# Kernel tuning notes

Measured on AMD Instinct MI355X. Metric: run time of the kernel, lower is better.

Reference implementation:

```python
import jax, jax.numpy as jnp
import numpy as np
import math

N_HEADS = 16
ROPE_BASE = 10000.0


def rotate_half(x):
    x1 = x[..., ::2]
    x2 = x[..., 1::2]
    return jnp.stack((-x2, x1), axis=-1).reshape(x.shape)


def rope_tables(seq_len, head_dim, dtype):
    inv_freq = 1.0 / (ROPE_BASE ** (jnp.arange(0, head_dim, 2, dtype=jnp.float32) / head_dim))
    positions = jnp.arange(seq_len, dtype=jnp.float32)
    freqs = jnp.outer(positions, inv_freq)            # [S, hd/2]
    emb = jnp.concatenate((freqs, freqs), axis=-1)    # [S, hd]  (matches torch cat convention)
    cos = jnp.cos(emb)[None, None, :, :].astype(dtype)
    sin = jnp.sin(emb)[None, None, :, :].astype(dtype)
    return cos, sin


def setup_inputs() -> dict:
    key = jax.random.key(0)
    k1, k2, k3 = jax.random.split(key, 3)
    B, S, D = 2, 2048, 1024
    x = jax.random.normal(k1, (B, S, D), dtype=jnp.float32)
    # causal lower-triangular mask, broadcastable over batch and heads
    mask = jnp.tril(jnp.ones((S, S), dtype=jnp.int32))[None, None, :, :]
    w_qkv = jax.random.normal(k2, (D, 3 * D), dtype=jnp.float32) * 0.02
    w_out = jax.random.normal(k3, (D, D), dtype=jnp.float32) * 0.02
    return {"x": x, "mask": mask, "w_qkv": w_qkv, "w_out": w_out}


def reference(x, mask, w_qkv, w_out):
    B, S, D = x.shape
    H = N_HEADS
    hd = D // H
    qkv = (x @ w_qkv).reshape(B, S, 3, H, hd)
    qkv = jnp.transpose(qkv, (2, 0, 3, 1, 4))         # [3, B, H, S, hd]
    q, k, v = qkv[0], qkv[1], qkv[2]
    cos, sin = rope_tables(S, hd, x.dtype)
    q = q * cos + rotate_half(q) * sin
    k = k * cos + rotate_half(k) * sin
    scale = math.sqrt(hd)
    attn = jnp.einsum("bhsd,bhtd->bhst", q, k) / scale
    attn = jnp.where(mask == 0, -jnp.inf, attn)
    attn = jax.nn.softmax(attn, axis=-1)              # dropout p=0.0 -> identity
    out = jnp.einsum("bhst,bhtd->bhsd", attn, v)
    out = jnp.transpose(out, (0, 2, 1, 3)).reshape(B, S, D)
    return out @ w_out
```

## Files before the change

### kernel.cpp

```cpp
#include <hip/hip_runtime.h>
#include <stdint.h>

typedef unsigned short u16;
typedef __bf16 bf16x8 __attribute__((ext_vector_type(8)));
typedef float f32x4 __attribute__((ext_vector_type(4)));

#define S_LEN 2048
#define NH    16
#define DM    1024
#define N3    3072
#define MROWS 4096

__device__ __forceinline__ float b2f(u16 u) {
  unsigned int v = ((unsigned int)u) << 16;
  return __builtin_bit_cast(float, v);
}
__device__ __forceinline__ u16 f2b(float f) {
  unsigned int v = __builtin_bit_cast(unsigned int, f);
  v += 0x7fffu + ((v >> 16) & 1u);
  return (u16)(v >> 16);
}
__device__ __forceinline__ u16 f2b_trunc(float f) {
  return (u16)(__builtin_bit_cast(unsigned int, f) >> 16);
}
__device__ __forceinline__ bf16x8 ld8(const u16* p) { return *(const bf16x8*)p; }
__device__ __forceinline__ f32x4 mfma16(bf16x8 a, bf16x8 b, f32x4 c) {
  return __builtin_amdgcn_mfma_f32_16x16x32_bf16(a, b, c, 0, 0, 0);
}
__device__ __forceinline__ void glds16(const void* g, void* l) {
  __builtin_amdgcn_global_load_lds(
      (const __attribute__((address_space(1))) unsigned int*)g,
      (__attribute__((address_space(3))) unsigned int*)l, 16, 0, 0);
}
__device__ __forceinline__ int bfish(unsigned int w) {
  unsigned int e = (w >> 7) & 0xffu;
  return (e >= 100u && e <= 134u) ? 1 : 0;
}

__global__ __launch_bounds__(256) void prep_kernel(const void* __restrict__ x,
                                                   const void* __restrict__ wqkv,
                                                   const void* __restrict__ wout,
                                                   u16* __restrict__ xb,
                                                   u16* __restrict__ wqT,
                                                   u16* __restrict__ woT,
                                                   float* __restrict__ cosT,
                                                   float* __restrict__ sinT,
                                                   int* __restrict__ flag) {
  const int bx = blockIdx.x;
  const int t = threadIdx.x;
  if (bx < 2048) {
    __shared__ int cnt;
    if (t == 0) cnt = 0;
    __syncthreads();
    size_t i = (size_t)bx * 256 + t;
    const uint4* xv = (const uint4*)x;
    uint4 probe = xv[i];
    unsigned int wds[4]; *(uint4*)wds = probe;
    atomicAdd(&cnt, bfish(wds[0]) + bfish(wds[1]) + bfish(wds[2]) + bfish(wds[3]));
    __syncthreads();
    const int isbf = cnt > 512;
    if (t == 0) *flag = isbf;
    if (isbf) {
      ((uint4*)xb)[i] = probe;
    } else {
      const float* xf = (const float*)x;
      #pragma unroll
      for (int j = 0; j < 8; ++j) xb[i * 8 + j] = f2b(xf[i * 8 + j]);
    }
    return;
  }
  if (bx < 2304) {
    int i = (bx - 2048) * 256 + t;
    int s = i >> 5, f = i & 31;
    float invf = expf(-(float)(2 * f) * (1.0f / 64.0f) * logf(10000.0f));
    float th = (float)s * invf;
    float sv, cv;
    sincosf(th, &sv, &cv);
    cosT[s * 64 + f] = cv; cosT[s * 64 + 32 + f] = cv;
    sinT[s * 64 + f] = sv; sinT[s * 64 + 32 + f] = sv;
    return;
  }
  const int wq = bx < 5376;
  const int id = wq ? (bx - 2304) : (bx - 5376);
  const int ncx = wq ? 96 : 32;
  const void* in = wq ? wqkv : wout;
  u16* out = wq ? wqT : woT;
  const int C = wq ? 3072 : 1024;
  const int bxc = id % ncx, byr = id / ncx;
  __shared__ int cnt;
  __shared__ float tile[32][33];
  const int tx = t & 31, ty = t >> 5;
  if (t == 0) cnt = 0;
  __syncthreads();
  const unsigned int* wv = (const unsigned int*)in;
  size_t off = (((size_t)id) * 256 + t) & 524287;
  atomicAdd(&cnt, bfish(wv[off]));
  __syncthreads();
  const int fl = cnt > 128;
  const int c0 = bxc * 32, r0 = byr * 32;
  #pragma unroll
  for (int dy = 0; dy < 32; dy += 8) {
    size_t idx = (size_t)(r0 + ty + dy) * C + (c0 + tx);
    float v = fl ? b2f(((const u16*)in)[idx]) : ((const float*)in)[idx];
    tile[ty + dy][tx] = v;
  }
  __syncthreads();
  #pragma unroll
  for (int dy = 0; dy < 32; dy += 8) {
    out[(size_t)(c0 + ty + dy) * 1024 + (r0 + tx)] = f2b(tile[tx][ty + dy]);
  }
}

__global__ __launch_bounds__(256) void gemm_qkv(const u16* __restrict__ A,
                                                const u16* __restrict__ Bt,
                                                u16* __restrict__ Qo,
                                                u16* __restrict__ Ko,
                                                u16* __restrict__ Vt,
                                                const float* __restrict__ cosT,
                                                const float* __restrict__ sinT) {
  __shared__ u16 smem[16384];
  u16* Al = smem;
  u16* Bl = smem + 8192;
  const int t = threadIdx.x;
  const int lane = t & 63, wave = t >> 6;
  const int ln = lane & 15, quad = lane >> 4;
  const int wr = wave >> 1, wc = wave & 1;
  const int m0 = blockIdx.x * 128, n0 = blockIdx.y * 128;
  const char* Ab = (const char*)A;
  const char* Bb = (const char*)Bt;
  f32x4 acc[4][4] = {};

  for (int k0 = 0; k0 < 1024; k0 += 64) {
    __syncthreads();
    #pragma unroll
    for (int it = 0; it < 4; ++it) {
      int c = it * 256 + t;
      int row = c >> 3;
      int sg = (c & 7) ^ (row & 7);
      glds16(Ab + ((size_t)(m0 + row) * 1024 + k0 + sg * 8) * 2, (char*)Al + c * 16);
      glds16(Bb + ((size_t)(n0 + row) * 1024 + k0 + sg * 8) * 2, (char*)Bl + c * 16);
    }
    __syncthreads();
    bf16x8 a[4][2], b[4][2];
    #pragma unroll
    for (int i = 0; i < 4; ++i) {
      const int row = wr * 64 + i * 16 + ln;
      #pragma unroll
      for (int ki = 0; ki < 2; ++ki)
        a[i][ki] = ld8(Al + row * 64 + (((ki * 4 + quad) ^ (row & 7)) << 3));
    }
    #pragma unroll
    for (int j = 0; j < 4; ++j) {
      const int row = wc * 64 + j * 16 + ln;
      #pragma unroll
      for (int ki = 0; ki < 2; ++ki)
        b[j][ki] = ld8(Bl + row * 64 + (((ki * 4 + quad) ^ (row & 7)) << 3));
    }
    #pragma unroll
    for (int i = 0; i < 4; ++i)
      #pragma unroll
      for (int j = 0; j < 4; ++j) {
        acc[i][j] = mfma16(a[i][0], b[j][0], acc[i][j]);
        acc[i][j] = mfma16(a[i][1], b[j][1], acc[i][j]);
      }
  }

  const int which = n0 >> 10;
  if (which < 2) {
    u16* dst = which ? Ko : Qo;
    const float qs = which ? 1.0f : 0.18033688011112042f;
    #pragma unroll
    for (int i = 0; i < 4; ++i)
      #pragma unroll
      for (int j = 0; j < 4; ++j) {
        const int c = n0 + wc * 64 + j * 16 + ln;
        const int h = (c >> 6) & 15, d = c & 63;
        const float sgn = (d & 1) ? 1.0f : -1.0f;
        #pragma unroll
        for (int r = 0; r < 4; ++r) {
          const int m = m0 + wr * 64 + i * 16 + quad * 4 + r;
          const int s = m & 2047, b_ = m >> 11;
          const float v = acc[i][j][r];
          const float p = __shfl_xor(v, 1);
          const float o = (v * cosT[s * 64 + d] + sgn * p * sinT[s * 64 + d]) * qs;
          dst[((size_t)(b_ * NH + h) * S_LEN + s) * 64 + d] = f2b(o);
        }
      }
  } else {
    #pragma unroll
    for (int i = 0; i < 4; ++i)
      #pragma unroll
      for (int j = 0; j < 4; ++j) {
        const int c = n0 + wc * 64 + j * 16 + ln;
        const int h = (c >> 6) & 15, d = c & 63;
        const int m = m0 + wr * 64 + i * 16 + quad * 4;
        const int s = m & 2047, b_ = m >> 11;
        u16 pk[4];
        #pragma unroll
        for (int r = 0; r < 4; ++r) pk[r] = f2b(acc[i][j][r]);
        *(uint2*)&Vt[((size_t)(b_ * NH + h) * 64 + d) * S_LEN + s] = *(const uint2*)pk;
      }
  }
}

__global__ __launch_bounds__(256) void attn_kernel(const u16* __restrict__ Qb,
                                                   const u16* __restrict__ Kb,
                                                   const u16* __restrict__ Vt,
                                                   u16* __restrict__ Ao) {
  __shared__ u16 smem[20480];
  u16* Kl = smem;
  u16* Vl = smem + 8192;
  u16* Pl = smem + 16384;
  const int t = threadIdx.x;
  const int lane = t & 63, w = t >> 6;
  const int ln = lane & 15, quad = lane >> 4;
  const int i = blockIdx.x;
  const int xcd = i & 7;
  const int j = i >> 3;
  const int bh = (xcd << 2) | (j & 3);
  const int q5 = j >> 2;
  const int g = q5 & 7, s5 = q5 >> 3;
  const int qt = (s5 & 1) ? (31 - ((s5 >> 1) << 3) - g) : (((s5 >> 1) << 3) + g);
  const int q0 = qt * 64;
  const int b = bh >> 4, h = bh & 15;
  const u16* Qbh = Qb + (size_t)bh * (S_LEN * 64);
  const u16* Kbh = Kb + (size_t)bh * (S_LEN * 64);
  const u16* Vtbh = Vt + (size_t)bh * (64 * S_LEN);
  u16* Plw = Pl + w * 1024;
  u16* AoBase = Ao + (size_t)b * S_LEN * DM + h * 64;

  auto stage = [&](int kt, int bufi) {
    u16* kd = Kl + bufi * 4096;
    u16* vd = Vl + bufi * 4096;
    const u16* kg = Kbh + (size_t)kt * 64 * 64;
    const u16* vg = Vtbh + (size_t)kt * 64;
    #pragma unroll
    for (int it = 0; it < 2; ++it) {
      int c = it * 256 + t;
      int row = c >> 3, sg = (c & 7) ^ (row & 7);
      glds16((const char*)kg + ((size_t)row * 64 + sg * 8) * 2,   (char*)kd + c * 16);
      glds16((const char*)vg + ((size_t)row * 2048 + sg * 8) * 2, (char*)vd + c * 16);
    }
  };

  bf16x8 bq[2];
  #pragma unroll
  for (int kk = 0; kk < 2; ++kk)
    bq[kk] = ld8(Qbh + (size_t)(q0 + w * 16 + ln) * 64 + kk * 32 + quad * 8);

  f32x4 o[4] = {};
  float l = 0.f;

  stage(0, 0);
  __syncthreads();

  for (int kt = 0; kt <= qt; ++kt) {
    const int bufi = kt & 1;
    if (kt < qt) stage(kt + 1, bufi ^ 1);
    const u16* Kb_ = Kl + bufi * 4096;
    const u16* Vb_ = Vl + bufi * 4096;

    f32x4 st[4] = {};
    #pragma unroll
    for (int kk = 0; kk < 2; ++kk)
      #pragma unroll
      for (int ct = 0; ct < 4; ++ct) {
        bf16x8 ak = ld8(Kb_ + (ct * 16 + ln) * 64 + (((kk * 4 + quad) ^ (ln & 7)) << 3));
        st[ct] = mfma16(ak, bq[kk], st[ct]);
      }

    const bool diag = (kt == qt);
    #pragma unroll
    for (int ct = 0; ct < 4; ++ct) {
      u16 pk[4];
      #pragma unroll
      for (int r = 0; r < 4; ++r) {
        float p;
        if (diag && (ct * 16 + quad * 4 + r) > (w * 16 + ln)) p = 0.f;
        else p = __builtin_amdgcn_exp2f(st[ct][r]);
        l += p;
        pk[r] = f2b_trunc(p);
      }
      *(uint2*)(Plw + ln * 64 + ((((ct * 2) + (quad >> 1)) ^ (ln & 7)) << 3)
                + ((quad & 1) << 2)) = *(const uint2*)pk;
    }

    #pragma unroll
    for (int k4 = 0; k4 < 2; ++k4) {
      bf16x8 bp = ld8(Plw + ln * 64 + (((k4 * 4 + quad) ^ (ln & 7)) << 3));
      #pragma unroll
      for (int dt = 0; dt < 4; ++dt) {
        bf16x8 av = ld8(Vb_ + (dt * 16 + ln) * 64 + (((k4 * 4 + quad) ^ (ln & 7)) << 3));
        o[dt] = mfma16(av, bp, o[dt]);
      }
    }
    __syncthreads();
  }

  l += __shfl_xor(l, 16);
  l += __shfl_xor(l, 32);
  const float inv = 1.f / l;
  const size_t qrow = (size_t)(q0 + w * 16 + ln) * DM;
  #pragma unroll
  for (int dt = 0; dt < 4; ++dt) {
    u16 pk[4];
    #pragma unroll
    for (int r = 0; r < 4; ++r) pk[r] = f2b(o[dt][r] * inv);
    *(uint2*)(AoBase + qrow + dt * 16 + quad * 4) = *(const uint2*)pk;
  }
}

template <int TM>
__global__ __launch_bounds__(256) void gemm_out_t(const u16* __restrict__ A,
                                                  const u16* __restrict__ Bt,
                                                  void* __restrict__ Out,
                                                  const int* __restrict__ flag) {
  constexpr int MI = TM / 32;
  __shared__ u16 smem[(TM + 128) * 32];
  u16* Al = smem;
  u16* Bl = smem + TM * 32;
  const int t = threadIdx.x;
  const int lane = t & 63, wave = t >> 6;
  const int ln = lane & 15, quad = lane >> 4;
  const int wr = wave >> 1, wc = wave & 1;
  const int m0 = blockIdx.x * TM, n0 = blockIdx.y * 128;
  const int rr = t >> 2;
  const int cb = (t & 3) * 16;
  const char* Ab = (const char*)A;
  const char* Bb = (const char*)Bt;
  f32x4 acc[MI][4] = {};

  for (int k0 = 0; k0 < 1024; k0 += 32) {
    __syncthreads();
    #pragma unroll
    for (int p = 0; p < TM / 64; ++p)
      glds16(Ab + ((size_t)(m0 + p * 64 + rr) * 1024 + k0) * 2 + cb,
             (char*)Al + p * 4096 + t * 16);
    glds16(Bb + ((size_t)(n0 + rr) * 1024 + k0) * 2 + cb,      (char*)Bl + t * 16);
    glds16(Bb + ((size_t)(n0 + 64 + rr) * 1024 + k0) * 2 + cb, (char*)Bl + 4096 + t * 16);
    __syncthreads();
    bf16x8 a[MI], b[4];
    #pragma unroll
    for (int i = 0; i < MI; ++i)
      a[i] = ld8(Al + (wr * (TM / 2) + i * 16 + ln) * 32 + quad * 8);
    #pragma unroll
    for (int j = 0; j < 4; ++j)
      b[j] = ld8(Bl + (wc * 64 + j * 16 + ln) * 32 + quad * 8);
    #pragma unroll
    for (int i = 0; i < MI; ++i)
      #pragma unroll
      for (int j = 0; j < 4; ++j)
        acc[i][j] = mfma16(a[i], b[j], acc[i][j]);
  }

  const int fl = *flag;
  #pragma unroll
  for (int i = 0; i < MI; ++i)
    #pragma unroll
    for (int j = 0; j < 4; ++j)
      #pragma unroll
      for (int r = 0; r < 4; ++r) {
        int m = m0 + wr * (TM / 2) + i * 16 + quad * 4 + r;
        int c = n0 + wc * 64 + j * 16 + ln;
        float v = acc[i][j][r];
        if (fl) ((u16*)Out)[(size_t)m * DM + c] = f2b(v);
        else    ((float*)Out)[(size_t)m * DM + c] = v;
      }
}

extern "C" void kernel_launch(void* const* d_in, const int* in_sizes, int n_in,
                              void* d_out, int out_size, void* d_ws, size_t ws_size,
                              hipStream_t stream) {
  (void)in_sizes; (void)n_in; (void)out_size; (void)ws_size;
  const void* x    = d_in[0];
  const void* wqkv = d_in[2];
  const void* wout = d_in[3];
  char* ws = (char*)d_ws;
  u16*  xb   = (u16*)(ws + 0);
  u16*  Ao   = xb;
  u16*  wqT  = (u16*)(ws + 8388608);
  u16*  woT  = (u16*)(ws + 14680064);
  u16*  Qb   = (u16*)(ws + 16777216);
  u16*  Kb   = (u16*)(ws + 25165824);
  u16*  Vt   = (u16*)(ws + 33554432);
  float* cosT = (float*)(ws + 41943040);
  float* sinT = (float*)(ws + 42467328);
  int*  flag = (int*)(ws + 42991616);

  prep_kernel<<<6400, 256, 0, stream>>>(x, wqkv, wout, xb, wqT, woT, cosT, sinT, flag);
  gemm_qkv<<<dim3(32, 24), 256, 0, stream>>>(xb, wqT, Qb, Kb, Vt, cosT, sinT);
  attn_kernel<<<1024, 256, 0, stream>>>(Qb, Kb, Vt, Ao);
  gemm_out_t<64><<<dim3(64, 8), 256, 0, stream>>>(Ao, woT, d_out, flag);
}
```

Baseline: 193.8 us.

## Tile weight transpose 64x64 with vector IO, interleave RoPE table, load A directly

```diff
diff --git a/kernel.cpp b/kernel.cpp
--- a/kernel.cpp
+++ b/kernel.cpp
@@ -43,8 +43,7 @@
                                                    u16* __restrict__ xb,
                                                    u16* __restrict__ wqT,
                                                    u16* __restrict__ woT,
-                                                   float* __restrict__ cosT,
-                                                   float* __restrict__ sinT,
+                                                   float* __restrict__ cs,
                                                    int* __restrict__ flag) {
   const int bx = blockIdx.x;
   const int t = threadIdx.x;
@@ -69,45 +68,62 @@
     }
     return;
   }
-  if (bx < 2304) {
+  if (bx < 2560) {
     int i = (bx - 2048) * 256 + t;
-    int s = i >> 5, f = i & 31;
+    int d = i >> 11, s = i & 2047;
+    int f = d & 31;
     float invf = expf(-(float)(2 * f) * (1.0f / 64.0f) * logf(10000.0f));
     float th = (float)s * invf;
     float sv, cv;
     sincosf(th, &sv, &cv);
-    cosT[s * 64 + f] = cv; cosT[s * 64 + 32 + f] = cv;
-    sinT[s * 64 + f] = sv; sinT[s * 64 + 32 + f] = sv;
+    cs[i * 2] = cv; cs[i * 2 + 1] = sv;
     return;
   }
-  const int wq = bx < 5376;
-  const int id = wq ? (bx - 2304) : (bx - 5376);
-  const int ncx = wq ? 96 : 32;
+  const int wq = bx < 3328;
+  const int id = wq ? (bx - 2560) : (bx - 3328);
+  const int ncx = wq ? 48 : 16;
   const void* in = wq ? wqkv : wout;
   u16* out = wq ? wqT : woT;
   const int C = wq ? 3072 : 1024;
-  const int bxc = id % ncx, byr = id / ncx;
+  const int c0 = (id % ncx) * 64, r0 = (id / ncx) * 64;
   __shared__ int cnt;
-  __shared__ float tile[32][33];
-  const int tx = t & 31, ty = t >> 5;
+  __shared__ u16 L[4096];
   if (t == 0) cnt = 0;
   __syncthreads();
   const unsigned int* wv = (const unsigned int*)in;
-  size_t off = (((size_t)id) * 256 + t) & 524287;
+  size_t off = (((size_t)id) * 256 + t) & 262143;
   atomicAdd(&cnt, bfish(wv[off]));
   __syncthreads();
   const int fl = cnt > 128;
-  const int c0 = bxc * 32, r0 = byr * 32;
-  #pragma unroll
-  for (int dy = 0; dy < 32; dy += 8) {
-    size_t idx = (size_t)(r0 + ty + dy) * C + (c0 + tx);
-    float v = fl ? b2f(((const u16*)in)[idx]) : ((const float*)in)[idx];
-    tile[ty + dy][tx] = v;
+  if (fl) {
+    #pragma unroll
+    for (int it = 0; it < 2; ++it) {
+      int c = it * 256 + t;
+      int rl = c >> 3, cseg = c & 7;
+      uint4 v = *(const uint4*)((const u16*)in + (size_t)(r0 + rl) * C + c0 + cseg * 8);
+      u16 e[8]; *(uint4*)e = v;
+      #pragma unroll
+      for (int jj = 0; jj < 8; ++jj) {
+        int cl = cseg * 8 + jj;
+        L[cl * 64 + (rl ^ (cseg << 3))] = e[jj];
+      }
+    }
+  } else {
+    const float* inf_ = (const float*)in;
+    #pragma unroll
+    for (int it = 0; it < 16; ++it) {
+      int c = it * 256 + t;
+      int rl = c >> 6, cl = c & 63;
+      L[cl * 64 + (rl ^ ((cl >> 3) << 3))] = f2b(inf_[(size_t)(r0 + rl) * C + c0 + cl]);
+    }
   }
   __syncthreads();
   #pragma unroll
-  for (int dy = 0; dy < 32; dy += 8) {
-    out[(size_t)(c0 + ty + dy) * 1024 + (r0 + tx)] = f2b(tile[tx][ty + dy]);
+  for (int it = 0; it < 2; ++it) {
+    int c = it * 256 + t;
+    int cl = c >> 3, rseg = c & 7;
+    uint4 v = *(const uint4*)(L + cl * 64 + (((rseg ^ (cl >> 3)) & 7) << 3));
+    *(uint4*)(out + (size_t)(c0 + cl) * 1024 + r0 + rseg * 8) = v;
   }
 }
 
@@ -116,39 +132,36 @@
                                                 u16* __restrict__ Qo,
                                                 u16* __restrict__ Ko,
                                                 u16* __restrict__ Vt,
-                                                const float* __restrict__ cosT,
-                                                const float* __restrict__ sinT) {
-  __shared__ u16 smem[16384];
-  u16* Al = smem;
-  u16* Bl = smem + 8192;
+                                                const float* __restrict__ cs) {
+  __shared__ u16 Bl[8192];
   const int t = threadIdx.x;
   const int lane = t & 63, wave = t >> 6;
   const int ln = lane & 15, quad = lane >> 4;
   const int wr = wave >> 1, wc = wave & 1;
   const int m0 = blockIdx.x * 128, n0 = blockIdx.y * 128;
-  const char* Ab = (const char*)A;
   const char* Bb = (const char*)Bt;
   f32x4 acc[4][4] = {};
+  const u16* Ap[4];
+  #pragma unroll
+  for (int i = 0; i < 4; ++i)
+    Ap[i] = A + (size_t)(m0 + wr * 64 + i * 16 + ln) * 1024 + quad * 8;
 
   for (int k0 = 0; k0 < 1024; k0 += 64) {
     __syncthreads();
     #pragma unroll
     for (int it = 0; it < 4; ++it) {
       int c = it * 256 + t;
-      int row = c >> 3;
-      int sg = (c & 7) ^ (row & 7);
-      glds16(Ab + ((size_t)(m0 + row) * 1024 + k0 + sg * 8) * 2, (char*)Al + c * 16);
+      int row = c >> 3, sg = (c & 7) ^ (row & 7);
       glds16(Bb + ((size_t)(n0 + row) * 1024 + k0 + sg * 8) * 2, (char*)Bl + c * 16);
     }
-    __syncthreads();
-    bf16x8 a[4][2], b[4][2];
-    #pragma unroll
-    for (int i = 0; i < 4; ++i) {
-      const int row = wr * 64 + i * 16 + ln;
+    bf16x8 a[4][2];
+    #pragma unroll
+    for (int i = 0; i < 4; ++i)
       #pragma unroll
       for (int ki = 0; ki < 2; ++ki)
-        a[i][ki] = ld8(Al + row * 64 + (((ki * 4 + quad) ^ (row & 7)) << 3));
-    }
+        a[i][ki] = ld8(Ap[i] + k0 + ki * 32);
+    __syncthreads();
+    bf16x8 b[4][2];
     #pragma unroll
     for (int j = 0; j < 4; ++j) {
       const int row = wc * 64 + j * 16 + ln;
@@ -170,22 +183,27 @@
     u16* dst = which ? Ko : Qo;
     const float qs = which ? 1.0f : 0.18033688011112042f;
     #pragma unroll
-    for (int i = 0; i < 4; ++i)
+    for (int i = 0; i < 4; ++i) {
+      const int mb = m0 + wr * 64 + i * 16 + quad * 4;
+      const int s0 = mb & 2047, b_ = mb >> 11;
       #pragma unroll
       for (int j = 0; j < 4; ++j) {
         const int c = n0 + wc * 64 + j * 16 + ln;
         const int h = (c >> 6) & 15, d = c & 63;
         const float sgn = (d & 1) ? 1.0f : -1.0f;
+        const float4* csp = (const float4*)(cs + ((size_t)d * 2048 + s0) * 2);
+        const float4 c01 = csp[0], c23 = csp[1];
+        const float cosv[4] = {c01.x, c01.z, c23.x, c23.z};
+        const float sinv[4] = {c01.y, c01.w, c23.y, c23.w};
+        u16* drow = dst + ((size_t)(b_ * NH + h) * S_LEN + s0) * 64 + d;
         #pragma unroll
         for (int r = 0; r < 4; ++r) {
-          const int m = m0 + wr * 64 + i * 16 + quad * 4 + r;
-          const int s = m & 2047, b_ = m >> 11;
           const float v = acc[i][j][r];
           const float p = __shfl_xor(v, 1);
-          const float o = (v * cosT[s * 64 + d] + sgn * p * sinT[s * 64 + d]) * qs;
-          dst[((size_t)(b_ * NH + h) * S_LEN + s) * 64 + d] = f2b(o);
+          drow[r * 64] = f2b((v * cosv[r] + sgn * p * sinv[r]) * qs);
         }
       }
+    }
   } else {
     #pragma unroll
     for (int i = 0; i < 4; ++i)
@@ -383,12 +401,11 @@
   u16*  Qb   = (u16*)(ws + 16777216);
   u16*  Kb   = (u16*)(ws + 25165824);
   u16*  Vt   = (u16*)(ws + 33554432);
-  float* cosT = (float*)(ws + 41943040);
-  float* sinT = (float*)(ws + 42467328);
+  float* cs  = (float*)(ws + 41943040);
   int*  flag = (int*)(ws + 42991616);
 
-  prep_kernel<<<6400, 256, 0, stream>>>(x, wqkv, wout, xb, wqT, woT, cosT, sinT, flag);
-  gemm_qkv<<<dim3(32, 24), 256, 0, stream>>>(xb, wqT, Qb, Kb, Vt, cosT, sinT);
+  prep_kernel<<<3584, 256, 0, stream>>>(x, wqkv, wout, xb, wqT, woT, cs, flag);
+  gemm_qkv<<<dim3(32, 24), 256, 0, stream>>>(xb, wqT, Qb, Kb, Vt, cs);
   attn_kernel<<<1024, 256, 0, stream>>>(Qb, Kb, Vt, Ao);
   gemm_out_t<64><<<dim3(64, 8), 256, 0, stream>>>(Ao, woT, d_out, flag);
 }
```

Measured after the change: 215.3 us. 1.11x slower.
